# Kernel tuning notes

Hardware: AMD Instinct MI355X
Metric: run time of the kernel (lower is better)

The kernel has to match this reference:

```python
import jax, jax.numpy as jnp
import numpy as np

EPS = 1e-5   # BatchNorm eps
TAU = 0.1    # gumbel-softmax temperature (self.temperature)
N_LOCAL = 32 # max_local_num
B, M, D, S = 4, 8192, 64, 1024
MLP = [32, 128]


def setup_inputs() -> dict:
    key = jax.random.key(0)
    ks = jax.random.split(key, 12)
    coordinate = jax.random.normal(ks[0], (B, M, 3), dtype=jnp.float32)
    feature = jax.random.normal(ks[1], (B, M, D), dtype=jnp.float32)
    u = jax.random.uniform(ks[2], (B, S, M), dtype=jnp.float32, minval=1e-6, maxval=1.0 - 1e-6)
    gumbel_noise = -jnp.log(-jnp.log(u))
    w0 = jax.random.normal(ks[3], (5, MLP[0]), dtype=jnp.float32) * (1.0 / np.sqrt(5))
    w1 = jax.random.normal(ks[4], (MLP[0], MLP[1]), dtype=jnp.float32) * (1.0 / np.sqrt(MLP[0]))
    w2 = jax.random.normal(ks[5], (MLP[1], S), dtype=jnp.float32) * (1.0 / np.sqrt(MLP[1]))
    bn0_gamma = 1.0 + 0.1 * jax.random.normal(ks[6], (MLP[0],), dtype=jnp.float32)
    bn0_beta = 0.1 * jax.random.normal(ks[7], (MLP[0],), dtype=jnp.float32)
    bn0_mean = 0.1 * jax.random.normal(ks[8], (MLP[0],), dtype=jnp.float32)
    bn0_var = jax.random.uniform(ks[9], (MLP[0],), dtype=jnp.float32, minval=0.5, maxval=1.5)
    bn1_gamma = 1.0 + 0.1 * jax.random.normal(ks[10], (MLP[1],), dtype=jnp.float32)
    bn1_beta = 0.1 * jax.random.normal(ks[11], (MLP[1],), dtype=jnp.float32)
    k2 = jax.random.split(jax.random.fold_in(key, 7), 2)
    bn1_mean = 0.1 * jax.random.normal(k2[0], (MLP[1],), dtype=jnp.float32)
    bn1_var = jax.random.uniform(k2[1], (MLP[1],), dtype=jnp.float32, minval=0.5, maxval=1.5)
    return dict(coordinate=coordinate, feature=feature, gumbel_noise=gumbel_noise,
                w0=w0, bn0_gamma=bn0_gamma, bn0_beta=bn0_beta, bn0_mean=bn0_mean, bn0_var=bn0_var,
                w1=w1, bn1_gamma=bn1_gamma, bn1_beta=bn1_beta, bn1_mean=bn1_mean, bn1_var=bn1_var,
                w2=w2)


def _bn(x, gamma, beta, mean, var):
    # BatchNorm1d in inference form over the channel (last) dim
    return (x - mean) * jax.lax.rsqrt(var + EPS) * gamma + beta


def reference(coordinate, feature, gumbel_noise,
              w0, bn0_gamma, bn0_beta, bn0_mean, bn0_var,
              w1, bn1_gamma, bn1_beta, bn1_mean, bn1_var,
              w2):
    # spherical features: [x, y, z, theta, phi] -> [B, m, 5]
    r = jnp.linalg.norm(coordinate, axis=-1)
    th = jnp.arccos(coordinate[..., 2] / r)
    fi = jnp.arctan2(coordinate[..., 1], coordinate[..., 0])
    c2 = jnp.concatenate([coordinate, th[..., None], fi[..., None]], axis=-1)
    # per-point MLP with BN + ReLU
    h = jax.nn.relu(_bn(c2 @ w0, bn0_gamma, bn0_beta, bn0_mean, bn0_var))
    h = jax.nn.relu(_bn(h @ w1, bn1_gamma, bn1_beta, bn1_mean, bn1_var))
    logits = h @ w2                        # [B, m, s]
    Q = jax.nn.sigmoid(jnp.swapaxes(logits, 1, 2))  # [B, s, m]
    # topk grouping over points
    _, idx = jax.lax.top_k(Q, N_LOCAL)     # [B, s, n]
    b_idx = jnp.arange(coordinate.shape[0])[:, None, None]
    grouped_points = coordinate[b_idx, idx]   # [B, s, n, 3]
    grouped_feature = feature[b_idx, idx]     # [B, s, n, d]
    # gumbel-softmax (hard, straight-through) sampling over points
    y_soft = jax.nn.softmax((Q + gumbel_noise) / TAU, axis=-1)
    hard_idx = jnp.argmax(y_soft, axis=-1)
    y_hard = jax.nn.one_hot(hard_idx, Q.shape[-1], dtype=Q.dtype)
    Qg = y_hard - jax.lax.stop_gradient(y_soft) + y_soft  # [B, s, m]
    sampled_points = Qg @ coordinate        # [B, s, 3]
    sampled_feature = Qg @ feature          # [B, s, d]
    grouped_feature = grouped_feature.at[:, :, 0, :].set(sampled_feature)
    return sampled_points, grouped_points, sampled_feature, grouped_feature, Qg
```

## Files before the change

### kernel.cpp

```cpp
#include <hip/hip_runtime.h>
#include <math.h>

#define Bd   4
#define Md   8192
#define Dd   64
#define Sd   1024
#define H0d  32
#define H1d  128

#define OFF_SP 0
#define OFF_GP 12288
#define OFF_SF 405504
#define OFF_GF 667648
#define OFF_QG 9056256

#define CAP 512

__device__ __forceinline__ unsigned f2u(float f) {
    unsigned v = __float_as_uint(f);
    return (v & 0x80000000u) ? ~v : (v | 0x80000000u);
}

__global__ __launch_bounds__(256) void k1_mlp(
    const float* __restrict__ coord,
    const float* __restrict__ w0,
    const float* __restrict__ g0, const float* __restrict__ be0,
    const float* __restrict__ mu0, const float* __restrict__ va0,
    const float* __restrict__ w1,
    const float* __restrict__ g1, const float* __restrict__ be1,
    const float* __restrict__ mu1, const float* __restrict__ va1,
    float* __restrict__ h1T)
{
    const int jg = blockIdx.x & 3;
    const int j0 = jg * 32;
    __shared__ double W1[H0d * 32];
    __shared__ double W0[5 * H0d];
    __shared__ double MU0[H0d], RS0[H0d], BE0[H0d];
    __shared__ double MU1[32], RS1[32], BE1[32];
    const int t = threadIdx.x;
    for (int e = t; e < H0d * 32; e += 256) {
        int i = e >> 5, jc = e & 31;
        W1[e] = (double)w1[i * H1d + j0 + jc];
    }
    if (t < 5 * H0d) W0[t] = (double)w0[t];
    if (t < H0d) {
        MU0[t] = (double)mu0[t];
        RS0[t] = (double)g0[t] / sqrt((double)va0[t] + 1e-5);
        BE0[t] = (double)be0[t];
    }
    if (t >= 192 && t < 224) {
        int j = t - 192;
        MU1[j] = (double)mu1[j0 + j];
        RS1[j] = (double)g1[j0 + j] / sqrt((double)va1[j0 + j] + 1e-5);
        BE1[j] = (double)be1[j0 + j];
    }
    __syncthreads();

    const int p = (blockIdx.x >> 2) * 256 + t;
    const double x = (double)coord[p * 3 + 0];
    const double y = (double)coord[p * 3 + 1];
    const double z = (double)coord[p * 3 + 2];
    const double r  = sqrt(x * x + y * y + z * z);
    const double th = acos(z / r);
    const double fi = atan2(y, x);

    double h0[H0d];
    #pragma unroll
    for (int i = 0; i < H0d; i++) {
        double a = x * W0[i] + y * W0[H0d + i] + z * W0[2 * H0d + i]
                 + th * W0[3 * H0d + i] + fi * W0[4 * H0d + i];
        a = (a - MU0[i]) * RS0[i] + BE0[i];
        h0[i] = a > 0.0 ? a : 0.0;
    }
    float* o = h1T + (size_t)(p >> 13) * (H1d * Md) + (p & (Md - 1));
    for (int jc = 0; jc < 32; jc += 2) {
        double a0 = 0.0, a1 = 0.0;
        #pragma unroll
        for (int i = 0; i < H0d; i++) {
            double h = h0[i];
            a0 += h * W1[i * 32 + jc];
            a1 += h * W1[i * 32 + jc + 1];
        }
        a0 = (a0 - MU1[jc]) * RS1[jc] + BE1[jc];             a0 = a0 > 0.0 ? a0 : 0.0;
        a1 = (a1 - MU1[jc + 1]) * RS1[jc + 1] + BE1[jc + 1]; a1 = a1 > 0.0 ? a1 : 0.0;
        o[(size_t)(j0 + jc) * Md]     = (float)a0;
        o[(size_t)(j0 + jc + 1) * Md] = (float)a1;
    }
}

__global__ __launch_bounds__(256, 4) void k2_gemm(
    const float* __restrict__ h1T,
    const float* __restrict__ w2,
    float* __restrict__ logits)
{
    __shared__ float As[32][128];
    __shared__ float Bs[32][128];
    const int bx = blockIdx.x, b = blockIdx.y;
    const int mtile = bx & 63, stile = bx >> 6;
    const int m0 = mtile * 128, s0 = stile * 128;
    const int t = threadIdx.x;
    const int tm = t & 15, tn = t >> 4;

    float acc[8][8] = {};

    for (int kt = 0; kt < 4; kt++) {
        const float* Ag = h1T + ((size_t)b * H1d + kt * 32) * Md + m0;
        const float* Bg = w2 + (size_t)(kt * 32) * Sd + s0;
        #pragma unroll
        for (int i = 0; i < 4; i++) {
            int idx = t + i * 256;
            int kk = idx >> 5, c = idx & 31;
            *(float4*)&As[kk][c * 4] = *(const float4*)&Ag[(size_t)kk * Md + c * 4];
            *(float4*)&Bs[kk][c * 4] = *(const float4*)&Bg[(size_t)kk * Sd + c * 4];
        }
        __syncthreads();

        #pragma unroll 8
        for (int k = 0; k < 32; k++) {
            float a_[8], b_[8];
            *(float4*)&a_[0] = *(const float4*)&As[k][tm * 4];
            *(float4*)&a_[4] = *(const float4*)&As[k][64 + tm * 4];
            *(float4*)&b_[0] = *(const float4*)&Bs[k][tn * 4];
            *(float4*)&b_[4] = *(const float4*)&Bs[k][64 + tn * 4];
            #pragma unroll
            for (int si = 0; si < 8; si++)
                #pragma unroll
                for (int mi = 0; mi < 8; mi++)
                    acc[si][mi] += b_[si] * a_[mi];
        }
        __syncthreads();
    }

    #pragma unroll
    for (int si = 0; si < 8; si++) {
        int s = s0 + (si >> 2) * 64 + tn * 4 + (si & 3);
        float* row = logits + ((size_t)b * Sd + s) * Md + m0;
        *(float4*)&row[tm * 4]      = make_float4(acc[si][0], acc[si][1], acc[si][2], acc[si][3]);
        *(float4*)&row[64 + tm * 4] = make_float4(acc[si][4], acc[si][5], acc[si][6], acc[si][7]);
    }
}

__global__ __launch_bounds__(256) void k3_fused(
    float* __restrict__ logits,
    const float* __restrict__ gumbel,
    const float* __restrict__ coord,
    const float* __restrict__ feat,
    float* __restrict__ out)
{
    const int r = blockIdx.x;
    const int b = r >> 10;
    const int t = threadIdx.x;
    const int lane = t & 63, wav = t >> 6;
    const float4* L4 = (const float4*)(logits + (size_t)r * Md);
    const float4* G4 = (const float4*)(gumbel + (size_t)r * Md);

    __shared__ unsigned long long wred[2][4];
    __shared__ unsigned long long ck[CAP];
    __shared__ unsigned swT[4];
    __shared__ int cnt;
    __shared__ int order[32];

    unsigned uq[32];
    unsigned gbu = 0u; int gbm = 0;
    #pragma unroll
    for (int j = 0; j < 8; j++) {
        float4 v = L4[j * 256 + t];
        float4 g = G4[j * 256 + t];
        #pragma unroll
        for (int c = 0; c < 4; c++) {
            float x = ((const float*)&v)[c];
            float q = 1.0f / (1.0f + expf(-x));
            uq[j * 4 + c] = f2u(q);
            unsigned us = f2u(q + ((const float*)&g)[c]);
            if (us > gbu) { gbu = us; gbm = j * 1024 + t * 4 + c; }
        }
    }

    {
        unsigned long long key = ((unsigned long long)gbu << 32) | (unsigned)(Md - 1 - gbm);
        #pragma unroll
        for (int o = 32; o > 0; o >>= 1) {
            unsigned long long other = __shfl_down(key, o);
            if (other > key) key = other;
        }
        if (lane == 0) wred[0][wav] = key;
    }
    if (t == 0) cnt = 0;
    __syncthreads();
    unsigned long long gbest = wred[0][0];
    if (wred[0][1] > gbest) gbest = wred[0][1];
    if (wred[0][2] > gbest) gbest = wred[0][2];
    if (wred[0][3] > gbest) gbest = wred[0][3];
    const int am = Md - 1 - (int)(gbest & 0xFFFFFFFFull);

    unsigned pm = 0u;
    #pragma unroll
    for (int i = 0; i < 32; i++) pm = max(pm, uq[i]);
    unsigned v = pm;
    #pragma unroll
    for (int k = 2; k <= 64; k <<= 1) {
        #pragma unroll
        for (int j = k >> 1; j > 0; j >>= 1) {
            unsigned o = __shfl_xor(v, j);
            bool up = ((lane & k) == 0);
            bool lower = ((lane & j) == 0);
            unsigned mn = min(v, o), mx = max(v, o);
            v = (lower == up) ? mn : mx;
        }
    }
    unsigned tw = __shfl(v, 32);
    if (lane == 0) swT[wav] = tw;
    __syncthreads();
    const unsigned T = max(max(swT[0], swT[1]), max(swT[2], swT[3]));

    #pragma unroll
    for (int i = 0; i < 32; i++) {
        if (uq[i] >= T) {
            int pos = atomicAdd(&cnt, 1);
            if (pos < CAP) {
                int m = (i >> 2) * 1024 + t * 4 + (i & 3);
                ck[pos] = ((unsigned long long)uq[i] << 32) | (unsigned)(Md - 1 - m);
            }
        }
    }
    __syncthreads();
    const int n = cnt;

    if (n >= 32 && n <= CAP) {
        for (int j2 = t; j2 < n; j2 += 256) {
            unsigned long long mine = ck[j2];
            int rk = 0;
            for (int i2 = 0; i2 < n; i2++) rk += (ck[i2] > mine) ? 1 : 0;
            if (rk < 32) order[rk] = Md - 1 - (int)(mine & 0xFFFFFFFFull);
        }
    } else {
        for (int round = 0; round < 32; round++) {
            unsigned bu = 0u; int bi = 0;
            #pragma unroll
            for (int i = 0; i < 32; i++)
                if (uq[i] > bu) { bu = uq[i]; bi = i; }
            int bm = (bi >> 2) * 1024 + t * 4 + (bi & 3);
            unsigned long long key =
                ((unsigned long long)bu << 32) | (unsigned)(Md - 1 - bm);
            #pragma unroll
            for (int o = 32; o > 0; o >>= 1) {
                unsigned long long other = __shfl_down(key, o);
                if (other > key) key = other;
            }
            const int p = round & 1;
            if (lane == 0) wred[p][wav] = key;
            __syncthreads();
            unsigned long long best = wred[p][0];
            if (wred[p][1] > best) best = wred[p][1];
            if (wred[p][2] > best) best = wred[p][2];
            if (wred[p][3] > best) best = wred[p][3];
            const int m_win = Md - 1 - (int)(best & 0xFFFFFFFFull);
            if (((m_win >> 2) & 255) == t)
                uq[(m_win >> 10) * 4 + (m_win & 3)] = 0u;
            if (t == 0) order[round] = m_win;
        }
    }
    __syncthreads();

    {
        const int q4 = am >> 2;
        float4* row = (float4*)(logits + (size_t)r * Md);
        #pragma unroll
        for (int i = 0; i < 8; i++) {
            int idx = i * 256 + t;
            float4 vv = make_float4(0.f, 0.f, 0.f, 0.f);
            if (idx == q4) ((float*)&vv)[am & 3] = 1.0f;
            row[idx] = vv;
        }
    }
    if (t < 3)
        out[OFF_SP + (size_t)r * 3 + t] = coord[((size_t)b * Md + am) * 3 + t];
    if (t >= 32 && t < 128) {
        int e = t - 32;
        int nn = e / 3, c = e - nn * 3;
        out[OFF_GP + (size_t)r * 96 + e] = coord[((size_t)b * Md + order[nn]) * 3 + c];
    }
    const float4* F4  = (const float4*)feat;
    float4* SF4 = (float4*)(out + OFF_SF);
    float4* GF4 = (float4*)(out + OFF_GF);
    if (t < 16) {
        float4 fv = F4[((size_t)b * Md + am) * 16 + t];
        SF4[(size_t)r * 16 + t]  = fv;
        GF4[(size_t)r * 512 + t] = fv;
    }
    for (int e4 = 16 + t; e4 < 512; e4 += 256) {
        int nn = e4 >> 4, d4 = e4 & 15;
        GF4[(size_t)r * 512 + e4] = F4[((size_t)b * Md + order[nn]) * 16 + d4];
    }
}

extern "C" void kernel_launch(void* const* d_in, const int* in_sizes, int n_in,
                              void* d_out, int out_size, void* d_ws, size_t ws_size,
                              hipStream_t stream)
{
    (void)in_sizes; (void)n_in; (void)out_size; (void)d_ws; (void)ws_size;
    const float* coord = (const float*)d_in[0];
    const float* feat  = (const float*)d_in[1];
    const float* gum   = (const float*)d_in[2];
    const float* w0    = (const float*)d_in[3];
    const float* g0    = (const float*)d_in[4];
    const float* be0   = (const float*)d_in[5];
    const float* mu0   = (const float*)d_in[6];
    const float* va0   = (const float*)d_in[7];
    const float* w1    = (const float*)d_in[8];
    const float* g1    = (const float*)d_in[9];
    const float* be1   = (const float*)d_in[10];
    const float* mu1   = (const float*)d_in[11];
    const float* va1   = (const float*)d_in[12];
    const float* w2    = (const float*)d_in[13];

    float*  out    = (float*)d_out;
    float*  h1T    = out + OFF_GF;
    float*  logits = out + OFF_QG;

    k1_mlp   <<<dim3(512),     dim3(256), 0, stream>>>(coord, w0, g0, be0, mu0, va0,
                                                       w1, g1, be1, mu1, va1, h1T);
    k2_gemm  <<<dim3(512, 4),  dim3(256), 0, stream>>>(h1T, w2, logits);
    k3_fused <<<dim3(4096),    dim3(256), 0, stream>>>(logits, gum, coord, feat, out);
}
```

Before: 218.0 us.

## Defer sigmoid to candidates; prefilter gumbel argmax by noise threshold

Instead of computing a sigmoid for all 32 elements per thread, the kernel selects top-k candidates on raw logits, since sigmoid is monotonic. It then applies sigmoid only to those candidates, with a safety check that falls back to the full path when candidates near the threshold may collide after rounding. The gumbel argmax is prefiltered to elements whose noise lies within about 1.01 of the row maximum (Q is bounded in [0,1]), and the exact key is computed only for those. This cuts transcendental work at the cost of more atomics, extra shared-memory state and reductions.

Measured after the change: 238.3 us. 9.3% more time.

```diff
diff --git a/kernel.cpp b/kernel.cpp
--- a/kernel.cpp
+++ b/kernel.cpp
@@ -19,6 +19,9 @@
 __device__ __forceinline__ unsigned f2u(float f) {
     unsigned v = __float_as_uint(f);
     return (v & 0x80000000u) ? ~v : (v | 0x80000000u);
+}
+__device__ __forceinline__ float u2f(unsigned u) {
+    return __uint_as_float((u & 0x80000000u) ? (u ^ 0x80000000u) : ~u);
 }
 
 __global__ __launch_bounds__(256) void k1_mlp(
@@ -156,46 +159,34 @@
 
     __shared__ unsigned long long wred[2][4];
     __shared__ unsigned long long ck[CAP];
-    __shared__ unsigned swT[4];
-    __shared__ int cnt;
+    __shared__ unsigned swT[4], swG[4], swNC[4];
+    __shared__ int cnt, gcnt;
+    __shared__ unsigned minQ32;
+    __shared__ unsigned long long gkey;
     __shared__ int order[32];
-
-    unsigned uq[32];
-    unsigned gbu = 0u; int gbm = 0;
+    __shared__ int   gm_lds[32];
+    __shared__ float gl_lds[32], gg_lds[32];
+
+    float lraw[32], graw[32];
     #pragma unroll
     for (int j = 0; j < 8; j++) {
         float4 v = L4[j * 256 + t];
         float4 g = G4[j * 256 + t];
         #pragma unroll
         for (int c = 0; c < 4; c++) {
-            float x = ((const float*)&v)[c];
-            float q = 1.0f / (1.0f + expf(-x));
-            uq[j * 4 + c] = f2u(q);
-            unsigned us = f2u(q + ((const float*)&g)[c]);
-            if (us > gbu) { gbu = us; gbm = j * 1024 + t * 4 + c; }
-        }
-    }
-
-    {
-        unsigned long long key = ((unsigned long long)gbu << 32) | (unsigned)(Md - 1 - gbm);
-        #pragma unroll
-        for (int o = 32; o > 0; o >>= 1) {
-            unsigned long long other = __shfl_down(key, o);
-            if (other > key) key = other;
-        }
-        if (lane == 0) wred[0][wav] = key;
-    }
-    if (t == 0) cnt = 0;
-    __syncthreads();
-    unsigned long long gbest = wred[0][0];
-    if (wred[0][1] > gbest) gbest = wred[0][1];
-    if (wred[0][2] > gbest) gbest = wred[0][2];
-    if (wred[0][3] > gbest) gbest = wred[0][3];
-    const int am = Md - 1 - (int)(gbest & 0xFFFFFFFFull);
-
-    unsigned pm = 0u;
-    #pragma unroll
-    for (int i = 0; i < 32; i++) pm = max(pm, uq[i]);
+            lraw[j * 4 + c] = ((const float*)&v)[c];
+            graw[j * 4 + c] = ((const float*)&g)[c];
+        }
+    }
+
+    unsigned gmx = 0u, pm = 0u;
+    #pragma unroll
+    for (int i = 0; i < 32; i++) {
+        gmx = max(gmx, f2u(graw[i]));
+        pm  = max(pm,  f2u(lraw[i]));
+    }
+    #pragma unroll
+    for (int o = 32; o > 0; o >>= 1) gmx = max(gmx, (unsigned)__shfl_xor(gmx, o));
     unsigned v = pm;
     #pragma unroll
     for (int k = 2; k <= 64; k <<= 1) {
@@ -209,31 +200,89 @@
         }
     }
     unsigned tw = __shfl(v, 32);
-    if (lane == 0) swT[wav] = tw;
+    if (lane == 0) { swT[wav] = tw; swG[wav] = gmx; }
+    if (t == 0) { cnt = 0; gcnt = 0; minQ32 = 0xFFFFFFFFu; gkey = 0ull; }
     __syncthreads();
     const unsigned T = max(max(swT[0], swT[1]), max(swT[2], swT[3]));
-
+    const float gthr = u2f(max(max(swG[0], swG[1]), max(swG[2], swG[3]))) - 1.01f;
+
+    unsigned ncmax = 0u;
     #pragma unroll
     for (int i = 0; i < 32; i++) {
-        if (uq[i] >= T) {
+        const int m = (i >> 2) * 1024 + t * 4 + (i & 3);
+        if (graw[i] >= gthr) {
+            int gp = atomicAdd(&gcnt, 1);
+            if (gp < 32) { gm_lds[gp] = m; gl_lds[gp] = lraw[i]; gg_lds[gp] = graw[i]; }
+        }
+        unsigned ul = f2u(lraw[i]);
+        if (ul >= T) {
             int pos = atomicAdd(&cnt, 1);
             if (pos < CAP) {
-                int m = (i >> 2) * 1024 + t * 4 + (i & 3);
-                ck[pos] = ((unsigned long long)uq[i] << 32) | (unsigned)(Md - 1 - m);
+                float q = 1.0f / (1.0f + expf(-lraw[i]));
+                ck[pos] = ((unsigned long long)f2u(q) << 32) | (unsigned)(Md - 1 - m);
             }
-        }
-    }
-    __syncthreads();
-    const int n = cnt;
-
-    if (n >= 32 && n <= CAP) {
+        } else {
+            ncmax = max(ncmax, ul);
+        }
+    }
+    #pragma unroll
+    for (int o = 32; o > 0; o >>= 1) ncmax = max(ncmax, (unsigned)__shfl_xor(ncmax, o));
+    if (lane == 0) swNC[wav] = ncmax;
+    __syncthreads();
+    const int n = cnt, ng = gcnt;
+
+    if (ng <= 32) {
+        if (t < ng) {
+            float q = 1.0f / (1.0f + expf(-gl_lds[t]));
+            unsigned long long k = ((unsigned long long)f2u(q + gg_lds[t]) << 32)
+                                 | (unsigned)(Md - 1 - gm_lds[t]);
+            atomicMax(&gkey, k);
+        }
+    } else {
+        unsigned long long kb = 0ull;
+        #pragma unroll
+        for (int i = 0; i < 32; i++) {
+            const int m = (i >> 2) * 1024 + t * 4 + (i & 3);
+            float q = 1.0f / (1.0f + expf(-lraw[i]));
+            unsigned long long k = ((unsigned long long)f2u(q + graw[i]) << 32)
+                                 | (unsigned)(Md - 1 - m);
+            if (k > kb) kb = k;
+        }
+        #pragma unroll
+        for (int o = 32; o > 0; o >>= 1) {
+            unsigned long long ok = __shfl_down(kb, o);
+            if (ok > kb) kb = ok;
+        }
+        if (lane == 0) atomicMax(&gkey, kb);
+    }
+
+    const bool tryfast = (n >= 32 && n <= CAP);
+    if (tryfast) {
         for (int j2 = t; j2 < n; j2 += 256) {
             unsigned long long mine = ck[j2];
             int rk = 0;
             for (int i2 = 0; i2 < n; i2++) rk += (ck[i2] > mine) ? 1 : 0;
-            if (rk < 32) order[rk] = Md - 1 - (int)(mine & 0xFFFFFFFFull);
-        }
-    } else {
+            if (rk < 32) {
+                order[rk] = Md - 1 - (int)(mine & 0xFFFFFFFFull);
+                atomicMin(&minQ32, (unsigned)(mine >> 32));
+            }
+        }
+    }
+    __syncthreads();
+    const int am = Md - 1 - (int)(gkey & 0xFFFFFFFFull);
+
+    bool safe = false;
+    if (tryfast) {
+        const unsigned xnc = max(max(swNC[0], swNC[1]), max(swNC[2], swNC[3]));
+        float xf = u2f(xnc);
+        unsigned qnc = f2u(1.0f / (1.0f + expf(-xf)));
+        safe = (qnc + 4u) < minQ32;
+    }
+
+    if (!safe) {
+        unsigned uq[32];
+        #pragma unroll
+        for (int i = 0; i < 32; i++) uq[i] = f2u(1.0f / (1.0f + expf(-lraw[i])));
         for (int round = 0; round < 32; round++) {
             unsigned bu = 0u; int bi = 0;
             #pragma unroll
```
